# Optimization experiments

Hardware: AMD Instinct MI355X
Metric: run time of the kernel (lower is better)

Reference implementation:

```python
import jax, jax.numpy as jnp
import numpy as np

IN_F = 4096
OUT_F = 4096
BATCH = 4096


def _dequantize(q, mn, mx):
    # Faithful to dequantize_to_float32: per-tensor affine using the *observed*
    # integer min/max of the stored tensor.
    q_min = q.min()
    q_max = q.max()
    scale = (mx - mn) / (q_max - q_min).astype(jnp.float32)
    return (q - q_min).astype(jnp.float32) * scale + mn


def setup_inputs() -> dict:
    key = jax.random.key(0)
    k1, k2, k3 = jax.random.split(key, 3)
    x = jax.random.normal(k1, (BATCH, IN_F), dtype=jnp.float32)
    # int8-valued weights/bias stored as int32 (same math; dequant uses tensor min/max)
    weight_q = jax.random.randint(k2, (OUT_F, IN_F), -128, 128, dtype=jnp.int32)
    bias_q = jax.random.randint(k3, (OUT_F,), -128, 128, dtype=jnp.int32)
    # per-tensor float range recorded at quantization time (original scales by 255 first,
    # so these ranges are on the scaled tensor; any floats work for correctness testing)
    weight_min = jnp.float32(-4.2)
    weight_max = jnp.float32(4.5)
    bias_min = jnp.float32(-1.3)
    bias_max = jnp.float32(1.1)
    return {
        "x": x,
        "weight_q": weight_q,
        "bias_q": bias_q,
        "weight_min": weight_min,
        "weight_max": weight_max,
        "bias_min": bias_min,
        "bias_max": bias_max,
    }


def reference(x, weight_q, bias_q, weight_min, weight_max, bias_min, bias_max):
    w = _dequantize(weight_q, weight_min, weight_max)   # [OUT_F, IN_F] fp32
    b = _dequantize(bias_q, bias_min, bias_max)         # [OUT_F] fp32
    # F.linear: x @ W^T + b
    return jnp.einsum("bi,oi->bo", x, w) + b
```

## Files before the change

### kernel.cpp

```cpp
#include <hip/hip_runtime.h>
#include <climits>

#define IN_F 4096
#define OUT_F 4096
#define BATCH 4096
#define NPART 1024

typedef __bf16 bf16x8 __attribute__((ext_vector_type(8)));
typedef float f32x4 __attribute__((ext_vector_type(4)));

__device__ __forceinline__ unsigned short f2bf_rne(float f) {
  unsigned int u = __float_as_uint(f);
  u += 0x7fffu + ((u >> 16) & 1u);
  return (unsigned short)(u >> 16);
}

__global__ __launch_bounds__(256) void k_conv(const float* __restrict__ x,
                                              const int* __restrict__ q,
                                              unsigned short* __restrict__ xb,
                                              unsigned short* __restrict__ qb,
                                              float* __restrict__ rowsum,
                                              int* __restrict__ pmin,
                                              int* __restrict__ pmax) {
  if (blockIdx.x < NPART) {
    const int n4 = (OUT_F * IN_F) / 4;
    const int stride = NPART * 256;
    int vmin = INT_MAX, vmax = INT_MIN;
    const int4* q4 = (const int4*)q;
    ushort4* qb4 = (ushort4*)qb;
    for (int i = blockIdx.x * 256 + threadIdx.x; i < n4; i += stride) {
      int4 v = q4[i];
      vmin = min(vmin, min(min(v.x, v.y), min(v.z, v.w)));
      vmax = max(vmax, max(max(v.x, v.y), max(v.z, v.w)));
      ushort4 h;
      h.x = f2bf_rne((float)v.x);
      h.y = f2bf_rne((float)v.y);
      h.z = f2bf_rne((float)v.z);
      h.w = f2bf_rne((float)v.w);
      qb4[i] = h;
    }
    for (int off = 32; off > 0; off >>= 1) {
      vmin = min(vmin, __shfl_down(vmin, off));
      vmax = max(vmax, __shfl_down(vmax, off));
    }
    __shared__ int rmin[4], rmax[4];
    const int wave = threadIdx.x >> 6;
    if ((threadIdx.x & 63) == 0) { rmin[wave] = vmin; rmax[wave] = vmax; }
    __syncthreads();
    if (threadIdx.x == 0) {
      pmin[blockIdx.x] = min(min(rmin[0], rmin[1]), min(rmin[2], rmin[3]));
      pmax[blockIdx.x] = max(max(rmax[0], rmax[1]), max(rmax[2], rmax[3]));
    }
  } else {
    const int wave = threadIdx.x >> 6;
    const int lane = threadIdx.x & 63;
    const int row = (blockIdx.x - NPART) * 4 + wave;
    const float4* xr = (const float4*)(x + (size_t)row * IN_F);
    ushort4* xbr = (ushort4*)(xb + (size_t)row * IN_F);
    float s = 0.f;
#pragma unroll
    for (int it = 0; it < IN_F / 4 / 64; ++it) {
      const int i = it * 64 + lane;
      float4 v = xr[i];
      s += (v.x + v.y) + (v.z + v.w);
      ushort4 h;
      h.x = f2bf_rne(v.x); h.y = f2bf_rne(v.y);
      h.z = f2bf_rne(v.z); h.w = f2bf_rne(v.w);
      xbr[i] = h;
    }
    for (int off = 32; off > 0; off >>= 1) s += __shfl_down(s, off);
    if (lane == 0) rowsum[row] = s;
  }
}

__global__ __launch_bounds__(256) void k_wmm(const int* __restrict__ q,
                                             int* __restrict__ pmin,
                                             int* __restrict__ pmax) {
  const int n4 = (OUT_F * IN_F) / 4;
  const int stride = gridDim.x * blockDim.x;
  int vmin = INT_MAX, vmax = INT_MIN;
  const int4* q4 = (const int4*)q;
  for (int i = blockIdx.x * blockDim.x + threadIdx.x; i < n4; i += stride) {
    int4 v = q4[i];
    vmin = min(vmin, min(min(v.x, v.y), min(v.z, v.w)));
    vmax = max(vmax, max(max(v.x, v.y), max(v.z, v.w)));
  }
  for (int off = 32; off > 0; off >>= 1) {
    vmin = min(vmin, __shfl_down(vmin, off));
    vmax = max(vmax, __shfl_down(vmax, off));
  }
  __shared__ int rmin[4], rmax[4];
  const int wave = threadIdx.x >> 6;
  if ((threadIdx.x & 63) == 0) { rmin[wave] = vmin; rmax[wave] = vmax; }
  __syncthreads();
  if (threadIdx.x == 0) {
    pmin[blockIdx.x] = min(min(rmin[0], rmin[1]), min(rmin[2], rmin[3]));
    pmax[blockIdx.x] = max(max(rmax[0], rmax[1]), max(rmax[2], rmax[3]));
  }
}

__global__ __launch_bounds__(256) void k_scal(const int* __restrict__ pmin,
                                              const int* __restrict__ pmax, int npart,
                                              const int* __restrict__ bq,
                                              const float* __restrict__ wmn,
                                              const float* __restrict__ wmx,
                                              const float* __restrict__ bmn,
                                              const float* __restrict__ bmx,
                                              float* __restrict__ scal) {
  int vmin = INT_MAX, vmax = INT_MIN;
  for (int i = threadIdx.x; i < npart; i += 256) {
    vmin = min(vmin, pmin[i]);
    vmax = max(vmax, pmax[i]);
  }
  int bmin = INT_MAX, bmaxv = INT_MIN;
  for (int i = threadIdx.x; i < OUT_F; i += 256) {
    int v = bq[i];
    bmin = min(bmin, v);
    bmaxv = max(bmaxv, v);
  }
  for (int off = 32; off > 0; off >>= 1) {
    vmin = min(vmin, __shfl_down(vmin, off));
    vmax = max(vmax, __shfl_down(vmax, off));
    bmin = min(bmin, __shfl_down(bmin, off));
    bmaxv = max(bmaxv, __shfl_down(bmaxv, off));
  }
  __shared__ int r[4][4];
  const int wave = threadIdx.x >> 6;
  if ((threadIdx.x & 63) == 0) {
    r[wave][0] = vmin; r[wave][1] = vmax; r[wave][2] = bmin; r[wave][3] = bmaxv;
  }
  __syncthreads();
  if (threadIdx.x == 0) {
    int qmin = min(min(r[0][0], r[1][0]), min(r[2][0], r[3][0]));
    int qmax = max(max(r[0][1], r[1][1]), max(r[2][1], r[3][1]));
    int qbmin = min(min(r[0][2], r[1][2]), min(r[2][2], r[3][2]));
    int qbmax = max(max(r[0][3], r[1][3]), max(r[2][3], r[3][3]));
    float ws = (*wmx - *wmn) / (float)(qmax - qmin);
    scal[0] = ws;
    scal[1] = *wmn - ws * (float)qmin;
    float bs = (*bmx - *bmn) / (float)(qbmax - qbmin);
    scal[2] = bs;
    scal[3] = *bmn - bs * (float)qbmin;
  }
}

__device__ __forceinline__ void load_lds16(const unsigned short* g, unsigned short* l) {
  __builtin_amdgcn_global_load_lds(
      (const __attribute__((address_space(1))) unsigned int*)g,
      (__attribute__((address_space(3))) unsigned int*)l, 16, 0, 0);
}

#define VMW(n) asm volatile("s_waitcnt vmcnt(" #n ")" ::: "memory")
#define LGKM0  asm volatile("s_waitcnt lgkmcnt(0)" ::: "memory")
#define CFENCE asm volatile("" ::: "memory")

__global__ __launch_bounds__(512, 2) void k_gemm(
    const unsigned short* __restrict__ A,
    const unsigned short* __restrict__ B,
    const int* __restrict__ bq,
    const float* __restrict__ rowsum,
    const float* __restrict__ scal,
    float* __restrict__ C) {
  __shared__ __align__(16) unsigned short As[4][8192];
  __shared__ __align__(16) unsigned short Bs[4][8192];

  const int tid = threadIdx.x;
  const int w = tid >> 6;
  const int lane = tid & 63;
  const int bm = blockIdx.x * 256;
  const int bn = blockIdx.y * 256;

  const int wm = (w & 1) * 128;
  const int wn = (w >> 1) * 64;
  const int r16 = lane & 15;
  const int q = lane >> 4;
  const int pc = (q ^ ((r16 >> 1) & 3)) * 8;

  const int cA0 = w * 128 + lane;
  const int rowS0 = cA0 >> 2;
  const int colS0 = ((cA0 & 3) ^ ((rowS0 >> 1) & 3)) * 8;
  const int cA1 = cA0 + 64;
  const int rowS1 = cA1 >> 2;
  const int colS1 = ((cA1 & 3) ^ ((rowS1 >> 1) & 3)) * 8;
  const unsigned short* srcA0 = A + (size_t)(bm + rowS0) * IN_F + colS0;
  const unsigned short* srcA1 = A + (size_t)(bm + rowS1) * IN_F + colS1;
  const unsigned short* srcB0 = B + (size_t)(bn + rowS0) * IN_F + colS0;
  const unsigned short* srcB1 = B + (size_t)(bn + rowS1) * IN_F + colS1;
  const int dst0 = w * 1024;
  const int dst1 = w * 1024 + 512;

  f32x4 acc[8][4] = {};

  const int NT = IN_F / 32;

#pragma unroll
  for (int t = 0; t < 3; ++t) {
    load_lds16(srcA0 + t * 32, &As[t][dst0]);
    load_lds16(srcA1 + t * 32, &As[t][dst1]);
    load_lds16(srcB0 + t * 32, &Bs[t][dst0]);
    load_lds16(srcB1 + t * 32, &Bs[t][dst1]);
  }
  VMW(8);
  __builtin_amdgcn_s_barrier();
  CFENCE;

  for (int t = 0; t < NT; ++t) {
    const int s = t & 3;
    const unsigned short* Asl = As[s];
    const unsigned short* Bsl = Bs[s];
    const int s3 = (t + 3) & 3;
    const int koff = (t + 3) * 32;
    const bool pf = (t + 3 < NT);

    bf16x8 afr[4], bfr[4];
#pragma unroll
    for (int i = 0; i < 4; ++i)
      afr[i] = *(const bf16x8*)&Asl[(wm + i * 16 + r16) * 32 + pc];
#pragma unroll
    for (int i = 0; i < 4; ++i)
      bfr[i] = *(const bf16x8*)&Bsl[(wn + i * 16 + r16) * 32 + pc];
    if (pf) {
      load_lds16(srcA0 + koff, &As[s3][dst0]);
      load_lds16(srcA1 + koff, &As[s3][dst1]);
    }
    CFENCE;
    __builtin_amdgcn_s_barrier();
    LGKM0;
    __builtin_amdgcn_s_setprio(1);
#pragma unroll
    for (int mi = 0; mi < 4; ++mi)
#pragma unroll
      for (int ni = 0; ni < 4; ++ni)
        acc[mi][ni] = __builtin_amdgcn_mfma_f32_16x16x32_bf16(afr[mi], bfr[ni], acc[mi][ni], 0, 0, 0);
    __builtin_amdgcn_s_setprio(0);
    __builtin_amdgcn_s_barrier();

    bf16x8 af2[4];
#pragma unroll
    for (int i = 0; i < 4; ++i)
      af2[i] = *(const bf16x8*)&Asl[(wm + 64 + i * 16 + r16) * 32 + pc];
    if (pf) {
      load_lds16(srcB0 + koff, &Bs[s3][dst0]);
      load_lds16(srcB1 + koff, &Bs[s3][dst1]);
    }
    CFENCE;
    __builtin_amdgcn_s_barrier();
    LGKM0;
    __builtin_amdgcn_s_setprio(1);
#pragma unroll
    for (int mi = 0; mi < 4; ++mi)
#pragma unroll
      for (int ni = 0; ni < 4; ++ni)
        acc[4 + mi][ni] = __builtin_amdgcn_mfma_f32_16x16x32_bf16(af2[mi], bfr[ni], acc[4 + mi][ni], 0, 0, 0);
    __builtin_amdgcn_s_setprio(0);

    if (t < NT - 3)       VMW(8);
    else if (t == NT - 3) VMW(4);
    else if (t == NT - 2) VMW(0);
    __builtin_amdgcn_s_barrier();
    CFENCE;
  }

  const float wsc = scal[0], wbe = scal[1], bsc = scal[2], bbe = scal[3];
#pragma unroll
  for (int ni = 0; ni < 4; ++ni) {
    const int gn = bn + wn + ni * 16 + r16;
    const float bdq = bsc * (float)bq[gn] + bbe;
#pragma unroll
    for (int mi = 0; mi < 8; ++mi) {
      const int gm0 = bm + wm + mi * 16 + q * 4;
#pragma unroll
      for (int r = 0; r < 4; ++r) {
        const int gm = gm0 + r;
        C[(size_t)gm * OUT_F + gn] = wsc * acc[mi][ni][r] + wbe * rowsum[gm] + bdq;
      }
    }
  }
}

__global__ void k_naive(const float* __restrict__ x, const int* __restrict__ wq,
                        const int* __restrict__ bq, const float* __restrict__ scal,
                        float* __restrict__ out) {
  const int o = blockIdx.x * blockDim.x + threadIdx.x;
  const int b = blockIdx.y;
  const float* xr = x + (size_t)b * IN_F;
  const int* wr = wq + (size_t)o * IN_F;
  float s = 0.f, sx = 0.f;
  for (int k = 0; k < IN_F; ++k) {
    float xv = xr[k];
    s += xv * (float)wr[k];
    sx += xv;
  }
  out[(size_t)b * OUT_F + o] =
      scal[0] * s + scal[1] * sx + scal[2] * (float)bq[o] + scal[3];
}

extern "C" void kernel_launch(void* const* d_in, const int* in_sizes, int n_in,
                              void* d_out, int out_size, void* d_ws, size_t ws_size,
                              hipStream_t stream) {
  const float* x = (const float*)d_in[0];
  const int* wq = (const int*)d_in[1];
  const int* bq = (const int*)d_in[2];
  const float* wmn = (const float*)d_in[3];
  const float* wmx = (const float*)d_in[4];
  const float* bmn = (const float*)d_in[5];
  const float* bmx = (const float*)d_in[6];
  float* out = (float*)d_out;

  char* ws = (char*)d_ws;
  float* scal = (float*)ws;
  int* pmin = (int*)(ws + 64);
  int* pmax = (int*)(ws + 64 + NPART * 4);
  float* rowsum = (float*)(ws + 64 + 2 * NPART * 4);
  unsigned short* xb = (unsigned short*)(ws + 32768);
  unsigned short* qb = xb + (size_t)BATCH * IN_F;
  const size_t needed = 32768 + (size_t)BATCH * IN_F * 2 + (size_t)OUT_F * IN_F * 2;

  if (ws_size >= needed) {
    k_conv<<<2 * NPART, 256, 0, stream>>>(x, wq, xb, qb, rowsum, pmin, pmax);
    k_scal<<<1, 256, 0, stream>>>(pmin, pmax, NPART, bq, wmn, wmx, bmn, bmx, scal);
    dim3 grid(BATCH / 256, OUT_F / 256);
    k_gemm<<<grid, 512, 0, stream>>>(xb, qb, bq, rowsum, scal, out);
  } else {
    k_wmm<<<NPART, 256, 0, stream>>>(wq, pmin, pmax);
    k_scal<<<1, 256, 0, stream>>>(pmin, pmax, NPART, bq, wmn, wmx, bmn, bmx, scal);
    k_naive<<<dim3(OUT_F / 256, BATCH), 256, 0, stream>>>(x, wq, bq, scal, out);
  }
}
```

Baseline: 313.4 us.

## Switch GEMM inner loop to 32x32x16 bf16 MFMA with single barrier phase

Replaces the 16x16x32 MFMA tiling (8x4 accumulators per wave) with 32x32x16 MFMA (4x2 f32x16 accumulators), changing the LDS fragment load pattern and epilogue row mapping to match. It also merges the two half-step compute phases into one, issuing both A and B prefetches together and dropping one barrier per k-step. The larger MFMA shape reduces LDS fragment reads per FLOP and instruction count, but changes register pressure and may add LDS bank conflicts with the existing swizzle.

```diff
diff --git a/kernel.cpp b/kernel.cpp
--- a/kernel.cpp
+++ b/kernel.cpp
@@ -8,6 +8,7 @@
 
 typedef __bf16 bf16x8 __attribute__((ext_vector_type(8)));
 typedef float f32x4 __attribute__((ext_vector_type(4)));
+typedef float f32x16 __attribute__((ext_vector_type(16)));
 
 __device__ __forceinline__ unsigned short f2bf_rne(float f) {
   unsigned int u = __float_as_uint(f);
@@ -172,9 +173,8 @@
 
   const int wm = (w & 1) * 128;
   const int wn = (w >> 1) * 64;
-  const int r16 = lane & 15;
-  const int q = lane >> 4;
-  const int pc = (q ^ ((r16 >> 1) & 3)) * 8;
+  const int arow = lane & 31;
+  const int khalf = lane >> 5;
 
   const int cA0 = w * 128 + lane;
   const int rowS0 = cA0 >> 2;
@@ -189,7 +189,7 @@
   const int dst0 = w * 1024;
   const int dst1 = w * 1024 + 512;
 
-  f32x4 acc[8][4] = {};
+  f32x16 acc[4][2] = {};
 
   const int NT = IN_F / 32;
 
@@ -212,46 +212,41 @@
     const int koff = (t + 3) * 32;
     const bool pf = (t + 3 < NT);
 
-    bf16x8 afr[4], bfr[4];
-#pragma unroll
-    for (int i = 0; i < 4; ++i)
-      afr[i] = *(const bf16x8*)&Asl[(wm + i * 16 + r16) * 32 + pc];
-#pragma unroll
-    for (int i = 0; i < 4; ++i)
-      bfr[i] = *(const bf16x8*)&Bsl[(wn + i * 16 + r16) * 32 + pc];
+    bf16x8 af[4][2], bf[2][2];
+#pragma unroll
+    for (int mi = 0; mi < 4; ++mi) {
+      const int r = wm + mi * 32 + arow;
+      const int sw = ((r >> 1) & 3);
+#pragma unroll
+      for (int kk = 0; kk < 2; ++kk)
+        af[mi][kk] = *(const bf16x8*)&Asl[r * 32 + ((kk * 2 + khalf) ^ sw) * 8];
+    }
+#pragma unroll
+    for (int ni = 0; ni < 2; ++ni) {
+      const int r = wn + ni * 32 + arow;
+      const int sw = ((r >> 1) & 3);
+#pragma unroll
+      for (int kk = 0; kk < 2; ++kk)
+        bf[ni][kk] = *(const bf16x8*)&Bsl[r * 32 + ((kk * 2 + khalf) ^ sw) * 8];
+    }
     if (pf) {
       load_lds16(srcA0 + koff, &As[s3][dst0]);
       load_lds16(srcA1 + koff, &As[s3][dst1]);
+      load_lds16(srcB0 + koff, &Bs[s3][dst0]);
+      load_lds16(srcB1 + koff, &Bs[s3][dst1]);
     }
     CFENCE;
     __builtin_amdgcn_s_barrier();
     LGKM0;
     __builtin_amdgcn_s_setprio(1);
 #pragma unroll
-    for (int mi = 0; mi < 4; ++mi)
-#pragma unroll
-      for (int ni = 0; ni < 4; ++ni)
-        acc[mi][ni] = __builtin_amdgcn_mfma_f32_16x16x32_bf16(afr[mi], bfr[ni], acc[mi][ni], 0, 0, 0);
-    __builtin_amdgcn_s_setprio(0);
-    __builtin_amdgcn_s_barrier();
-
-    bf16x8 af2[4];
-#pragma unroll
-    for (int i = 0; i < 4; ++i)
-      af2[i] = *(const bf16x8*)&Asl[(wm + 64 + i * 16 + r16) * 32 + pc];
-    if (pf) {
-      load_lds16(srcB0 + koff, &Bs[s3][dst0]);
-      load_lds16(srcB1 + koff, &Bs[s3][dst1]);
-    }
-    CFENCE;
-    __builtin_amdgcn_s_barrier();
-    LGKM0;
-    __builtin_amdgcn_s_setprio(1);
-#pragma unroll
-    for (int mi = 0; mi < 4; ++mi)
-#pragma unroll
-      for (int ni = 0; ni < 4; ++ni)
-        acc[4 + mi][ni] = __builtin_amdgcn_mfma_f32_16x16x32_bf16(af2[mi], bfr[ni], acc[4 + mi][ni], 0, 0, 0);
+    for (int kk = 0; kk < 2; ++kk)
+#pragma unroll
+      for (int mi = 0; mi < 4; ++mi)
+#pragma unroll
+        for (int ni = 0; ni < 2; ++ni)
+          acc[mi][ni] = __builtin_amdgcn_mfma_f32_32x32x16_bf16(
+              af[mi][kk], bf[ni][kk], acc[mi][ni], 0, 0, 0);
     __builtin_amdgcn_s_setprio(0);
 
     if (t < NT - 3)       VMW(8);
@@ -262,16 +257,17 @@
   }
 
   const float wsc = scal[0], wbe = scal[1], bsc = scal[2], bbe = scal[3];
-#pragma unroll
-  for (int ni = 0; ni < 4; ++ni) {
-    const int gn = bn + wn + ni * 16 + r16;
+  const int rhi = khalf * 4;
+#pragma unroll
+  for (int ni = 0; ni < 2; ++ni) {
+    const int gn = bn + wn + ni * 32 + arow;
     const float bdq = bsc * (float)bq[gn] + bbe;
 #pragma unroll
-    for (int mi = 0; mi < 8; ++mi) {
-      const int gm0 = bm + wm + mi * 16 + q * 4;
-#pragma unroll
-      for (int r = 0; r < 4; ++r) {
-        const int gm = gm0 + r;
+    for (int mi = 0; mi < 4; ++mi) {
+      const int gm0 = bm + wm + mi * 32 + rhi;
+#pragma unroll
+      for (int r = 0; r < 16; ++r) {
+        const int gm = gm0 + (r & 3) + 8 * (r >> 2);
         C[(size_t)gm * OUT_F + gn] = wsc * acc[mi][ni][r] + wbe * rowsum[gm] + bdq;
       }
     }
```

Result: slower. 324.0 us (+3.4%).
